# Optimization experiments

Measured on AMD Instinct MI355X. Metric: run time of the kernel, lower is better.

## Reference

```python
import jax, jax.numpy as jnp
import numpy as np

B, L, H, C, K, S = 8, 336, 192, 321, 16, 8
H2 = H // 2 + 1            # rfft bins of pred_len
OUT = H2 * (2 * K + 1)     # FilterFactory out_dim


def _instance_norm(t):
    mu = t.mean(-1, keepdims=True)
    tc = t - mu
    std = jnp.sqrt((tc * tc).mean(-1, keepdims=True) + 1e-8)
    return tc / std, mu, std


def setup_inputs() -> dict:
    key = jax.random.key(0)
    ks = jax.random.split(key, 16)
    x = jax.random.normal(ks[0], (B, L, C), jnp.float32)
    y_hat = jax.random.normal(ks[1], (B, H, C), jnp.float32)
    leader_ids = jax.random.randint(ks[2], (B, C, K), 0, C)
    shift = jax.random.randint(ks[3], (B, C, K), 0, L)
    r = jax.random.normal(ks[4], (B, C, K), jnp.float32)
    temperature = jnp.ones((1,), jnp.float32)
    sl = 1.0 / np.sqrt(L)
    cls_w = jax.random.uniform(ks[5], (S, L), jnp.float32, -sl, sl)
    cls_bias = jax.random.uniform(ks[6], (S,), jnp.float32, -sl, sl)
    ss = 1.0 / np.sqrt(S)
    basic_state = jax.random.uniform(ks[7], (C, S), jnp.float32, -ss, ss)
    sk = 1.0 / np.sqrt(K)
    mh_w = jax.random.uniform(ks[8], (S, K * OUT), jnp.float32, -sk, sk)
    mh_b = jax.random.uniform(ks[9], (S, OUT), jnp.float32, -sk, sk)
    sm = 1.0 / np.sqrt(3 * H2)
    mix_w_real = jax.random.uniform(ks[10], (H2, 3 * H2), jnp.float32, -sm, sm)
    mix_w_imag = jax.random.uniform(ks[11], (H2, 3 * H2), jnp.float32, -sm, sm)
    mix_b_real = jax.random.uniform(ks[12], (H2,), jnp.float32, -sm, sm)
    mix_b_imag = jax.random.uniform(ks[13], (H2,), jnp.float32, -sm, sm)
    return dict(x=x, y_hat=y_hat, leader_ids=leader_ids, shift=shift, r=r,
                temperature=temperature, cls_w=cls_w, cls_bias=cls_bias,
                basic_state=basic_state, mh_w=mh_w, mh_b=mh_b,
                mix_w_real=mix_w_real, mix_w_imag=mix_w_imag,
                mix_b_real=mix_b_real, mix_b_imag=mix_b_imag)


def reference(x, y_hat, leader_ids, shift, r, temperature, cls_w, cls_bias,
              basic_state, mh_w, mh_b, mix_w_real, mix_w_imag,
              mix_b_real, mix_b_imag):
    xc = jnp.transpose(x, (0, 2, 1))        # [B,C,L]
    yh = jnp.transpose(y_hat, (0, 2, 1))    # [B,C,H]
    xn, mu, std = _instance_norm(xc)
    yhn = (yh - mu) / std

    # ---- shifted leader gather (no-grad region in original) ----
    seq = jnp.concatenate([xn, yhn], -1)                                      # [B,C,L+H]
    lead = jnp.take_along_axis(seq[:, None], leader_ids[..., None], axis=2)   # [B,C,K,L+H]
    idx = jnp.arange(L, L + H)[None, None, None, :] - shift[..., None]        # [B,C,K,H]
    seq_shifted = jnp.take_along_axis(lead, idx, axis=-1)
    seq_shifted = jax.lax.stop_gradient(seq_shifted * jnp.sign(r)[..., None])

    # ---- temperature softmax over [1, |r|] ----
    ones = jnp.ones((xc.shape[0], C, 1), xc.dtype)
    rw = jax.nn.softmax(jnp.concatenate([ones, jnp.abs(r)], -1) / temperature, axis=-1)
    corr_feat = rw[..., 1:]                                                   # [B,C,K]

    # ---- FilterFactory: state-routed filters ----
    p = jax.nn.softmax(cls_bias + basic_state + jnp.einsum('bcl,sl->bcs', xc, cls_w), axis=-1)
    w = jnp.einsum('bcs,so->bco', p, mh_w).reshape(-1, C, K, OUT)
    b = jnp.einsum('bcs,so->bco', p, mh_b)
    filt = (jnp.einsum('bck,bcko->bco', corr_feat, w) + b).reshape(-1, C, 2 * K + 1, H2)

    # ---- FFT filter mixing ----
    yf = jnp.fft.rfft(yhn)                                  # [B,C,H2] complex64
    sf = jnp.fft.rfft(seq_shifted) * filt[:, :, :K]         # [B,C,K,H2]
    df = (sf - yf[:, :, None]) * filt[:, :, K:-1]
    yf2 = yf * filt[:, :, -1]
    mix_in = jnp.concatenate([sf.sum(2), df.sum(2), yf2], -1)  # [B,C,3*H2]
    mix_w = mix_w_real + 1j * mix_w_imag
    mix_b = mix_b_real + 1j * mix_b_imag
    y = yhn + jnp.fft.irfft(mix_in @ mix_w.T + mix_b, n=H)
    y = y * std + mu
    return jnp.transpose(y, (0, 2, 1))                       # [B,H,C]
```

## Files before the change

kernel.cpp:

```cpp
#include <hip/hip_runtime.h>
#include <math.h>

#define B_ 8
#define L_ 336
#define H_ 192
#define C_ 321
#define K_ 16
#define S_ 8
#define H2_ 97
#define OUT_ 3201
#define SEQLEN_ 528
#define BC_ (B_ * C_)
#define JD_ 136
#define MIXJ_ 291
#define NP_ 208
#define MROWS_ 43656
#define MPAD_ 43712
#define NBLK_ 683
#define KF_ 160
#define MPADF_ 2576
#define NPADF_ 3264

typedef float v2f __attribute__((ext_vector_type(2)));
typedef float v4f __attribute__((ext_vector_type(4)));
typedef __attribute__((ext_vector_type(8))) short bf16x8;
typedef __attribute__((ext_vector_type(4))) float f32x4;

#define TWO_PI_F 6.283185307179586f

static constexpr size_t OFF_SEQ    = 0;
static constexpr size_t OFF_MU     = OFF_SEQ + (size_t)BC_ * SEQLEN_;
static constexpr size_t OFF_STD    = OFF_MU + BC_;
static constexpr size_t OFF_WT2    = (OFF_STD + BC_ + 3) & ~(size_t)3;
static constexpr size_t OFF_BPHI   = (OFF_WT2 + (size_t)2 * MIXJ_ * H2_ + 3) & ~(size_t)3;
static constexpr size_t OFF_BPLO   = OFF_BPHI + (size_t)NP_ * 192 / 2;
static constexpr size_t OFF_UHI    = (OFF_BPLO + (size_t)NP_ * 192 / 2 + 3) & ~(size_t)3;
static constexpr size_t OFF_ULO    = OFF_UHI + (size_t)MPADF_ * KF_ / 2;
static constexpr size_t OFF_W2HI   = OFF_ULO + (size_t)MPADF_ * KF_ / 2;
static constexpr size_t OFF_W2LO   = OFF_W2HI + (size_t)NPADF_ * KF_ / 2;
static constexpr size_t OFF_ROWS   = OFF_W2LO + (size_t)NPADF_ * KF_ / 2;
static constexpr size_t OFF_ROWSLO = OFF_ROWS + (size_t)MPAD_ * 192 / 2;
static constexpr size_t OFF_F      = OFF_ROWSLO + (size_t)MPAD_ * 192 / 2;
static constexpr size_t OFF_FILT   = OFF_ROWS;

__device__ inline void split_bf16(float v, unsigned short& hh, unsigned short& ll) {
  unsigned u = __float_as_uint(v);
  unsigned hb = (u + 0x7FFFu + ((u >> 16) & 1u)) & 0xFFFF0000u;
  float fh = __uint_as_float(hb);
  float fl = v - fh;
  unsigned u2 = __float_as_uint(fl);
  unsigned lb = (u2 + 0x7FFFu + ((u2 >> 16) & 1u)) >> 16;
  hh = (unsigned short)(hb >> 16);
  ll = (unsigned short)lb;
}

__launch_bounds__(256)
__global__ void kStats(const float* __restrict__ x, const float* __restrict__ cls_w,
                       const float* __restrict__ cls_bias,
                       const float* __restrict__ basic_state, const float* __restrict__ r,
                       const float* __restrict__ temperature,
                       float* __restrict__ mu, float* __restrict__ stdv,
                       unsigned short* __restrict__ uhi, unsigned short* __restrict__ ulo) {
  __shared__ float part[4][10][64];
  __shared__ float sp[64][S_];
  __shared__ float scf[64][K_];

  int b = blockIdx.x;
  int cb = blockIdx.y * 64;
  int lane = threadIdx.x & 63;
  int wv = threadIdx.x >> 6;
  int c = cb + lane;
  bool cok = c < C_;

  float sum = 0.f, sumsq = 0.f, a[S_];
#pragma unroll
  for (int s = 0; s < S_; s++) a[s] = 0.f;
  if (cok) {
    for (int l = wv * 84; l < wv * 84 + 84; l++) {
      float v = x[((size_t)b * L_ + l) * C_ + c];
      sum += v;
      sumsq = fmaf(v, v, sumsq);
#pragma unroll
      for (int s = 0; s < S_; s++) a[s] = fmaf(v, cls_w[s * L_ + l], a[s]);
    }
  }
  part[wv][0][lane] = sum;
  part[wv][1][lane] = sumsq;
#pragma unroll
  for (int s = 0; s < S_; s++) part[wv][2 + s][lane] = a[s];
  __syncthreads();

  if (threadIdx.x < 64 && cok) {
    float s0 = 0.f, s1 = 0.f, ac[S_];
#pragma unroll
    for (int s = 0; s < S_; s++) ac[s] = 0.f;
#pragma unroll
    for (int w = 0; w < 4; w++) {
      s0 += part[w][0][lane];
      s1 += part[w][1][lane];
#pragma unroll
      for (int s = 0; s < S_; s++) ac[s] += part[w][2 + s][lane];
    }
    float m = s0 * (1.f / L_);
    float var = fmaxf(s1 * (1.f / L_) - m * m, 0.f);
    float sd = sqrtf(var + 1e-8f);
    int bc = b * C_ + c;
    mu[bc] = m;
    stdv[bc] = sd;

    float lg[S_], mx = -1e30f;
#pragma unroll
    for (int s = 0; s < S_; s++) {
      lg[s] = ac[s] + cls_bias[s] + basic_state[c * S_ + s];
      mx = fmaxf(mx, lg[s]);
    }
    float den = 0.f;
#pragma unroll
    for (int s = 0; s < S_; s++) { float e = expf(lg[s] - mx); lg[s] = e; den += e; }
    float iden = 1.f / den;
#pragma unroll
    for (int s = 0; s < S_; s++) sp[lane][s] = lg[s] * iden;

    float it = 1.f / temperature[0];
    float aa[K_], am = it;
#pragma unroll
    for (int k = 0; k < K_; k++) {
      aa[k] = fabsf(r[(size_t)bc * K_ + k]) * it;
      am = fmaxf(am, aa[k]);
    }
    float den2 = expf(it - am);
#pragma unroll
    for (int k = 0; k < K_; k++) { float e = expf(aa[k] - am); aa[k] = e; den2 += e; }
    float iden2 = 1.f / den2;
#pragma unroll
    for (int k = 0; k < K_; k++) scf[lane][k] = aa[k] * iden2;
  }
  __syncthreads();

  for (int idx = threadIdx.x; idx < 64 * KF_; idx += 256) {
    int ci = idx / KF_;
    int j = idx - ci * KF_;
    if (cb + ci < C_) {
      float v = 0.f;
      if (j < JD_) {
        int s = j / 17;
        int t = j - s * 17;
        v = sp[ci][s];
        if (t < K_) v *= scf[ci][t];
      }
      unsigned short hh, ll;
      split_bf16(v, hh, ll);
      size_t row = (size_t)(b * C_ + cb + ci) * KF_ + j;
      uhi[row] = hh;
      ulo[row] = ll;
    }
  }
}

__launch_bounds__(256)
__global__ void kSeqT(const float* __restrict__ x, const float* __restrict__ y_hat,
                      const float* __restrict__ mu, const float* __restrict__ stdv,
                      float* __restrict__ seq) {
  __shared__ float tile[32][33];
  int b = blockIdx.x;
  int cb = blockIdx.y * 32;
  int tb = blockIdx.z * 32;
  int ci = threadIdx.x & 31;
  int q8 = threadIdx.x >> 5;
  int c = cb + ci;
  float m = 0.f, is = 0.f;
  if (c < C_) {
    m = mu[b * C_ + c];
    is = 1.f / stdv[b * C_ + c];
  }
#pragma unroll
  for (int q = 0; q < 4; q++) {
    int tt = q8 + q * 8;
    int t = tb + tt;
    float v = 0.f;
    if (c < C_ && t < SEQLEN_)
      v = (t < L_) ? x[((size_t)b * L_ + t) * C_ + c]
                   : y_hat[((size_t)b * H_ + (t - L_)) * C_ + c];
    tile[ci][tt] = (v - m) * is;
  }
  __syncthreads();
#pragma unroll
  for (int q = 0; q < 4; q++) {
    int cc = cb + q8 + q * 8;
    int t = tb + ci;
    if (cc < C_ && t < SEQLEN_)
      seq[((size_t)b * C_ + cc) * SEQLEN_ + t] = tile[q8 + q * 8][ci];
  }
}

__global__ void kPackB(unsigned short* __restrict__ bhi, unsigned short* __restrict__ blo) {
  int idx = blockIdx.x * 256 + threadIdx.x;
  if (idx >= NP_ * 192) return;
  int n = idx / 192;
  int h = idx - n * 192;
  float val = 0.f;
  if (n < H2_) {
    int ph = (n * h) % 192;
    val = cosf((TWO_PI_F / 192.f) * (float)ph);
  } else if (n >= 104 && n < 104 + H2_) {
    int ph = ((n - 104) * h) % 192;
    val = -sinf((TWO_PI_F / 192.f) * (float)ph);
  }
  unsigned short hh, ll;
  split_bf16(val, hh, ll);
  bhi[idx] = hh;
  blo[idx] = ll;
}

__global__ void kPackW2(const float* __restrict__ mh_w, const float* __restrict__ mh_b,
                        unsigned short* __restrict__ w2hi, unsigned short* __restrict__ w2lo) {
  int idx = blockIdx.x * 256 + threadIdx.x;
  if (idx >= NPADF_ * KF_) return;
  int n = idx / KF_;
  int k = idx - n * KF_;
  float v = 0.f;
  if (n < OUT_ && k < JD_) {
    int s = k / 17;
    int t = k - s * 17;
    v = (t < K_) ? mh_w[(size_t)s * (K_ * OUT_) + (size_t)t * OUT_ + n]
                 : mh_b[(size_t)s * OUT_ + n];
  }
  unsigned short hh, ll;
  split_bf16(v, hh, ll);
  w2hi[idx] = hh;
  w2lo[idx] = ll;
}

__global__ void kPackMixW(const float* __restrict__ mwr, const float* __restrict__ mwi,
                          float2* __restrict__ wT2) {
  int idx = blockIdx.x * blockDim.x + threadIdx.x;
  if (idx >= MIXJ_ * H2_) return;
  int j = idx / H2_;
  int g = idx - j * H2_;
  wT2[idx] = make_float2(mwr[(size_t)g * MIXJ_ + j], mwi[(size_t)g * MIXJ_ + j]);
}

__launch_bounds__(128)
__global__ void kGather(const float* __restrict__ seq, const int* __restrict__ lead,
                        const int* __restrict__ shiftv, const float* __restrict__ r,
                        unsigned short* __restrict__ rhi, unsigned short* __restrict__ rlo) {
  int bc = blockIdx.x;
  int b = bc / C_;
  int lane = threadIdx.x;
#pragma unroll 1
  for (int k = 0; k < 17; k++) {
    float sg;
    const float* src;
    if (k < K_) {
      int ld = lead[(size_t)bc * K_ + k];
      int sh = shiftv[(size_t)bc * K_ + k];
      float rv = r[(size_t)bc * K_ + k];
      sg = (rv > 0.f) ? 1.f : ((rv < 0.f) ? -1.f : 0.f);
      src = seq + ((size_t)b * C_ + ld) * SEQLEN_ + (L_ - sh);
    } else {
      sg = 1.f;
      src = seq + (size_t)bc * SEQLEN_ + L_;
    }
    size_t mrow = (size_t)(bc * 17 + k) * 192;
#pragma unroll
    for (int p = 0; p < 2; p++) {
      int h = lane + p * 128;
      if (h < H_) {
        float v = src[h] * sg;
        unsigned short hh, ll;
        split_bf16(v, hh, ll);
        rhi[mrow + h] = hh;
        rlo[mrow + h] = ll;
      }
    }
  }
}

__launch_bounds__(256)
__global__ void kDFT(const unsigned short* __restrict__ rhi,
                     const unsigned short* __restrict__ rlo,
                     const unsigned short* __restrict__ bhi,
                     const unsigned short* __restrict__ blo,
                     float* __restrict__ F) {
  __shared__ __align__(16) unsigned short Bs[52 * 512];
  int tid = threadIdx.x;
  int wv = tid >> 6;
  int lane = tid & 63;
  int m0 = blockIdx.x * 64 + wv * 16;
  int row = lane & 15;
  int kg = lane >> 4;

  f32x4 acc[13];
#pragma unroll
  for (int nt = 0; nt < 13; nt++) acc[nt] = (f32x4){0.f, 0.f, 0.f, 0.f};

  const unsigned short* Ahb = rhi + (size_t)(m0 + row) * 192 + kg * 8;
  const unsigned short* Alb = rlo + (size_t)(m0 + row) * 192 + kg * 8;

#pragma unroll 1
  for (int part = 0; part < 3; part++) {
    __syncthreads();
    for (int s = tid >> 6; s < 52; s += 4) {
      int plane = s & 1;
      int ntks = s >> 1;
      int nt = ntks >> 1;
      int ks2 = ntks & 1;
      const unsigned short* src = (plane ? blo : bhi)
          + (size_t)(nt * 16 + row) * 192 + part * 64 + ks2 * 32 + kg * 8;
      *(bf16x8*)(Bs + s * 512 + lane * 8) = *(const bf16x8*)src;
    }
    __syncthreads();
#pragma unroll
    for (int ks2 = 0; ks2 < 2; ks2++) {
      int ksg = part * 2 + ks2;
      bf16x8 ah = *(const bf16x8*)(Ahb + ksg * 32);
      bf16x8 al = *(const bf16x8*)(Alb + ksg * 32);
#pragma unroll
      for (int nt = 0; nt < 13; nt++) {
        bf16x8 bh = *(const bf16x8*)(Bs + ((nt * 2 + ks2) * 2 + 0) * 512 + lane * 8);
        bf16x8 bl = *(const bf16x8*)(Bs + ((nt * 2 + ks2) * 2 + 1) * 512 + lane * 8);
        acc[nt] = __builtin_amdgcn_mfma_f32_16x16x32_bf16(ah, bh, acc[nt], 0, 0, 0);
        acc[nt] = __builtin_amdgcn_mfma_f32_16x16x32_bf16(ah, bl, acc[nt], 0, 0, 0);
        acc[nt] = __builtin_amdgcn_mfma_f32_16x16x32_bf16(al, bh, acc[nt], 0, 0, 0);
      }
    }
  }

  int crow0 = m0 + kg * 4;
#pragma unroll
  for (int nt = 0; nt < 13; nt++) {
#pragma unroll
    for (int rr = 0; rr < 4; rr++) {
      F[(size_t)(crow0 + rr) * NP_ + nt * 16 + row] = acc[nt][rr];
    }
  }
}

__launch_bounds__(256)
__global__ void kFiltMM(const unsigned short* __restrict__ uhi,
                        const unsigned short* __restrict__ ulo,
                        const unsigned short* __restrict__ w2hi,
                        const unsigned short* __restrict__ w2lo,
                        float* __restrict__ filt) {
  __shared__ __align__(16) unsigned short Ws[40 * 512];
  int tid = threadIdx.x;
  int wv = tid >> 6;
  int lane = tid & 63;
  int m0 = (blockIdx.y * 4 + wv) * 16;
  int n0 = blockIdx.x * 64;
  int col = lane & 15;
  int kg = lane >> 4;

  for (int s = tid >> 6; s < 40; s += 4) {
    int plane = s & 1;
    int ntk = s >> 1;
    int nt = ntk / 5;
    int ksi = ntk - nt * 5;
    const unsigned short* src = (plane ? w2lo : w2hi)
        + (size_t)(n0 + nt * 16 + col) * KF_ + ksi * 32 + kg * 8;
    *(bf16x8*)(Ws + s * 512 + lane * 8) = *(const bf16x8*)src;
  }
  __syncthreads();

  f32x4 acc[4];
#pragma unroll
  for (int nt = 0; nt < 4; nt++) acc[nt] = (f32x4){0.f, 0.f, 0.f, 0.f};

  int mrow = (m0 + col < MPADF_) ? (m0 + col) : (MPADF_ - 1);
  const unsigned short* Ah = uhi + (size_t)mrow * KF_ + kg * 8;
  const unsigned short* Al = ulo + (size_t)mrow * KF_ + kg * 8;

#pragma unroll
  for (int ks = 0; ks < 5; ks++) {
    bf16x8 ah = *(const bf16x8*)(Ah + ks * 32);
    bf16x8 al = *(const bf16x8*)(Al + ks * 32);
#pragma unroll
    for (int nt = 0; nt < 4; nt++) {
      bf16x8 bh = *(const bf16x8*)(Ws + ((nt * 5 + ks) * 2 + 0) * 512 + lane * 8);
      bf16x8 bl = *(const bf16x8*)(Ws + ((nt * 5 + ks) * 2 + 1) * 512 + lane * 8);
      acc[nt] = __builtin_amdgcn_mfma_f32_16x16x32_bf16(ah, bh, acc[nt], 0, 0, 0);
      acc[nt] = __builtin_amdgcn_mfma_f32_16x16x32_bf16(ah, bl, acc[nt], 0, 0, 0);
      acc[nt] = __builtin_amdgcn_mfma_f32_16x16x32_bf16(al, bh, acc[nt], 0, 0, 0);
    }
  }

  int crow0 = m0 + kg * 4;
#pragma unroll
  for (int nt = 0; nt < 4; nt++) {
    int o = n0 + nt * 16 + col;
    if (o < OUT_) {
#pragma unroll
      for (int rr = 0; rr < 4; rr++) {
        int m = crow0 + rr;
        if (m < BC_) filt[(size_t)m * OUT_ + o] = acc[nt][rr];
      }
    }
  }
}

__launch_bounds__(256)
__global__ void kPost2(const float* __restrict__ F, const float* __restrict__ filt,
                       const float* __restrict__ seq,
                       const float* __restrict__ mu, const float* __restrict__ stdv,
                       const float2* __restrict__ wT2,
                       const float* __restrict__ mbr, const float* __restrict__ mbi,
                       float* __restrict__ out) {
  __shared__ __align__(16) v2f mix2[8][292];
  __shared__ float zrL[8][100], ziL[8][100];

  int tid = threadIdx.x;
  int half = tid >> 7;
  int ff = tid & 127;
  int bc0 = blockIdx.x * 8;

#pragma unroll 1
  for (int p = 0; p < 4; p++) {
    int bl = p * 2 + half;
    int bc = bc0 + bl;
    if (ff < H2_) {
      float Fre[17], Fim[17];
#pragma unroll
      for (int k = 0; k < 17; k++) {
        size_t mr = (size_t)(bc * 17 + k) * NP_;
        Fre[k] = F[mr + ff];
        Fim[k] = F[mr + 104 + ff];
      }
      const float* fb = filt + (size_t)bc * OUT_;
      float yfR = Fre[16], yfI = Fim[16];
      float S1r = 0.f, S1i = 0.f, S2r = 0.f, S2i = 0.f, sg2 = 0.f;
#pragma unroll
      for (int k = 0; k < K_; k++) {
        float g1 = fb[k * H2_ + ff];
        float g2 = fb[(K_ + k) * H2_ + ff];
        float g12 = g1 * g2;
        S1r = fmaf(Fre[k], g1, S1r);
        S1i = fmaf(Fim[k], g1, S1i);
        S2r = fmaf(Fre[k], g12, S2r);
        S2i = fmaf(Fim[k], g12, S2i);
        sg2 += g2;
      }
      S2r = fmaf(-yfR, sg2, S2r);
      S2i = fmaf(-yfI, sg2, S2i);
      float g3 = fb[32 * H2_ + ff];
      mix2[bl][ff] = (v2f){S1r, S1i};
      mix2[bl][H2_ + ff] = (v2f){S2r, S2i};
      mix2[bl][2 * H2_ + ff] = (v2f){yfR * g3, yfI * g3};
    }
  }
  __syncthreads();

  if (ff < H2_) {
    int g = ff;
    float zr_[4], zi_[4];
#pragma unroll
    for (int q = 0; q < 4; q++) { zr_[q] = mbr[g]; zi_[q] = mbi[g]; }
    const float2* wg = wT2 + g;
#pragma unroll 1
    for (int j = 0; j + 2 <= MIXJ_; j += 2) {
      float2 w0 = wg[(size_t)j * H2_];
      float2 w1 = wg[(size_t)(j + 1) * H2_];
#pragma unroll
      for (int q = 0; q < 4; q++) {
        v4f mm = *(const v4f*)&mix2[half * 4 + q][j];
        zr_[q] = fmaf(mm.x, w0.x, fmaf(-mm.y, w0.y, zr_[q]));
        zi_[q] = fmaf(mm.x, w0.y, fmaf(mm.y, w0.x, zi_[q]));
        zr_[q] = fmaf(mm.z, w1.x, fmaf(-mm.w, w1.y, zr_[q]));
        zi_[q] = fmaf(mm.z, w1.y, fmaf(mm.w, w1.x, zi_[q]));
      }
    }
    {
      int j = MIXJ_ - 1;
      float2 w0 = wg[(size_t)j * H2_];
#pragma unroll
      for (int q = 0; q < 4; q++) {
        v2f m2 = mix2[half * 4 + q][j];
        zr_[q] = fmaf(m2.x, w0.x, fmaf(-m2.y, w0.y, zr_[q]));
        zi_[q] = fmaf(m2.x, w0.y, fmaf(m2.y, w0.x, zi_[q]));
      }
    }
#pragma unroll
    for (int q = 0; q < 4; q++) {
      zrL[half * 4 + q][g] = zr_[q];
      ziL[half * 4 + q][g] = zi_[q];
    }
  }
  __syncthreads();

  if (ff < 96) {
    int h = ff;
    float ang = (TWO_PI_F / 192.f) * (float)h;
    float cs, sn;
    sincosf(ang, &sn, &cs);
#pragma unroll 1
    for (int q = 0; q < 4; q++) {
      int bl = half * 4 + q;
      int bc = bc0 + bl;
      int b = bc / C_;
      int c = bc - b * C_;
      float m = mu[bc], sd = stdv[bc];
      float base = 0.5f * zrL[bl][0] + ((h & 1) ? -0.5f : 0.5f) * zrL[bl][96];
      float aE = 0.f, aO = 0.f;
      float cv = cs, sv = sn;
      for (int fq = 1; fq < 96; fq += 2) {
        aO = fmaf(zrL[bl][fq], cv, fmaf(-ziL[bl][fq], sv, aO));
        float nc = cv * cs - sv * sn;
        float ns = cv * sn + sv * cs;
        aE = fmaf(zrL[bl][fq + 1], nc, fmaf(-ziL[bl][fq + 1], ns, aE));
        cv = nc * cs - ns * sn;
        sv = nc * sn + ns * cs;
      }
      float y0 = (base + aE + aO) * (2.f / 192.f);
      float y1 = (base + aE - aO) * (2.f / 192.f);
      const float* sq = seq + (size_t)bc * SEQLEN_ + L_;
      out[((size_t)b * H_ + h) * C_ + c] = fmaf(sq[h] + y0, sd, m);
      out[((size_t)b * H_ + h + 96) * C_ + c] = fmaf(sq[h + 96] + y1, sd, m);
    }
  }
}

extern "C" void kernel_launch(void* const* d_in, const int* in_sizes, int n_in,
                              void* d_out, int out_size, void* d_ws, size_t ws_size,
                              hipStream_t stream) {
  const float* x           = (const float*)d_in[0];
  const float* y_hat       = (const float*)d_in[1];
  const int*   lead        = (const int*)d_in[2];
  const int*   shiftv      = (const int*)d_in[3];
  const float* r           = (const float*)d_in[4];
  const float* temperature = (const float*)d_in[5];
  const float* cls_w       = (const float*)d_in[6];
  const float* cls_bias    = (const float*)d_in[7];
  const float* basic_state = (const float*)d_in[8];
  const float* mh_w        = (const float*)d_in[9];
  const float* mh_b        = (const float*)d_in[10];
  const float* mwr         = (const float*)d_in[11];
  const float* mwi         = (const float*)d_in[12];
  const float* mbr         = (const float*)d_in[13];
  const float* mbi         = (const float*)d_in[14];
  float* out = (float*)d_out;
  float* ws  = (float*)d_ws;

  unsigned short* bphi = (unsigned short*)(ws + OFF_BPHI);
  unsigned short* bplo = (unsigned short*)(ws + OFF_BPLO);
  unsigned short* uhi  = (unsigned short*)(ws + OFF_UHI);
  unsigned short* ulo  = (unsigned short*)(ws + OFF_ULO);
  unsigned short* w2hi = (unsigned short*)(ws + OFF_W2HI);
  unsigned short* w2lo = (unsigned short*)(ws + OFF_W2LO);
  unsigned short* rhi  = (unsigned short*)(ws + OFF_ROWS);
  unsigned short* rlo  = (unsigned short*)(ws + OFF_ROWSLO);

  dim3 gS(B_, 6);
  kStats<<<gS, 256, 0, stream>>>(x, cls_w, cls_bias, basic_state, r, temperature,
                                 ws + OFF_MU, ws + OFF_STD, uhi, ulo);

  dim3 gT(B_, 11, 17);
  kSeqT<<<gT, 256, 0, stream>>>(x, y_hat, ws + OFF_MU, ws + OFF_STD, ws + OFF_SEQ);

  kPackB<<<(NP_ * 192 + 255) / 256, 256, 0, stream>>>(bphi, bplo);

  kPackW2<<<(NPADF_ * KF_ + 255) / 256, 256, 0, stream>>>(mh_w, mh_b, w2hi, w2lo);

  kPackMixW<<<(MIXJ_ * H2_ + 255) / 256, 256, 0, stream>>>(
      mwr, mwi, (float2*)(ws + OFF_WT2));

  kGather<<<BC_, 128, 0, stream>>>(ws + OFF_SEQ, lead, shiftv, r, rhi, rlo);

  kDFT<<<NBLK_, 256, 0, stream>>>(rhi, rlo, bphi, bplo, ws + OFF_F);

  dim3 gFM(NPADF_ / 64, (MPADF_ / 16 + 3) / 4);
  kFiltMM<<<gFM, 256, 0, stream>>>(uhi, ulo, w2hi, w2lo, ws + OFF_FILT);

  kPost2<<<BC_ / 8, 256, 0, stream>>>(ws + OFF_F, ws + OFF_FILT, ws + OFF_SEQ,
                                      ws + OFF_MU, ws + OFF_STD,
                                      (const float2*)(ws + OFF_WT2), mbr, mbi, out);
}
```

Baseline: 255.5 us.

## Replace scalar mix and irfft post-kernel with split-bf16 MFMA GEMMs

Splits the fused post-processing kernel into four stages: a combine kernel that builds the complex mix inputs as split hi/lo bf16 rows, an MFMA GEMM applying the complex mixing weights (bias folded in as an extra K column), a second MFMA GEMM doing the irfft as a precomputed cosine/sine matrix, and a transposing epilogue that writes coalesced output. The goal is to replace the scalar FMA complex matmul and the per-thread rotation-recurrence inverse DFT with matrix-core work. The cost is extra kernel launches, intermediate round trips through global memory, and three-term bf16 split precision in place of fp32.

```diff
diff --git a/kernel.cpp b/kernel.cpp
--- a/kernel.cpp
+++ b/kernel.cpp
@@ -14,12 +14,15 @@
 #define JD_ 136
 #define MIXJ_ 291
 #define NP_ 208
-#define MROWS_ 43656
 #define MPAD_ 43712
 #define NBLK_ 683
 #define KF_ 160
 #define MPADF_ 2576
 #define NPADF_ 3264
+#define KMX_ 608
+#define NMX_ 208
+#define KIR_ 224
+#define NIR_ 192
 
 typedef float v2f __attribute__((ext_vector_type(2)));
 typedef float v4f __attribute__((ext_vector_type(4)));
@@ -31,8 +34,7 @@
 static constexpr size_t OFF_SEQ    = 0;
 static constexpr size_t OFF_MU     = OFF_SEQ + (size_t)BC_ * SEQLEN_;
 static constexpr size_t OFF_STD    = OFF_MU + BC_;
-static constexpr size_t OFF_WT2    = (OFF_STD + BC_ + 3) & ~(size_t)3;
-static constexpr size_t OFF_BPHI   = (OFF_WT2 + (size_t)2 * MIXJ_ * H2_ + 3) & ~(size_t)3;
+static constexpr size_t OFF_BPHI   = (OFF_STD + BC_ + 3) & ~(size_t)3;
 static constexpr size_t OFF_BPLO   = OFF_BPHI + (size_t)NP_ * 192 / 2;
 static constexpr size_t OFF_UHI    = (OFF_BPLO + (size_t)NP_ * 192 / 2 + 3) & ~(size_t)3;
 static constexpr size_t OFF_ULO    = OFF_UHI + (size_t)MPADF_ * KF_ / 2;
@@ -42,6 +44,15 @@
 static constexpr size_t OFF_ROWSLO = OFF_ROWS + (size_t)MPAD_ * 192 / 2;
 static constexpr size_t OFF_F      = OFF_ROWSLO + (size_t)MPAD_ * 192 / 2;
 static constexpr size_t OFF_FILT   = OFF_ROWS;
+static constexpr size_t OFF_MWHI   = OFF_F + (size_t)MPAD_ * NP_;
+static constexpr size_t OFF_MWLO   = OFF_MWHI + (size_t)NMX_ * KMX_ / 2;
+static constexpr size_t OFF_THI    = OFF_MWLO + (size_t)NMX_ * KMX_ / 2;
+static constexpr size_t OFF_TLO    = OFF_THI + (size_t)NIR_ * KIR_ / 2;
+static constexpr size_t OFF_MXHI   = OFF_TLO + (size_t)NIR_ * KIR_ / 2;
+static constexpr size_t OFF_MXLO   = OFF_MXHI + (size_t)MPADF_ * KMX_ / 2;
+static constexpr size_t OFF_ZHI    = OFF_MXLO + (size_t)MPADF_ * KMX_ / 2;
+static constexpr size_t OFF_ZLO    = OFF_ZHI + (size_t)MPADF_ * KIR_ / 2;
+static constexpr size_t OFF_Y      = OFF_ZLO + (size_t)MPADF_ * KIR_ / 2;
 
 __device__ inline void split_bf16(float v, unsigned short& hh, unsigned short& ll) {
   unsigned u = __float_as_uint(v);
@@ -231,13 +242,53 @@
   w2lo[idx] = ll;
 }
 
-__global__ void kPackMixW(const float* __restrict__ mwr, const float* __restrict__ mwi,
-                          float2* __restrict__ wT2) {
-  int idx = blockIdx.x * blockDim.x + threadIdx.x;
-  if (idx >= MIXJ_ * H2_) return;
-  int j = idx / H2_;
-  int g = idx - j * H2_;
-  wT2[idx] = make_float2(mwr[(size_t)g * MIXJ_ + j], mwi[(size_t)g * MIXJ_ + j]);
+__global__ void kPackMixW2(const float* __restrict__ mwr, const float* __restrict__ mwi,
+                           const float* __restrict__ mbr, const float* __restrict__ mbi,
+                           unsigned short* __restrict__ mwhi, unsigned short* __restrict__ mwlo) {
+  int idx = blockIdx.x * 256 + threadIdx.x;
+  if (idx >= NMX_ * KMX_) return;
+  int n = idx / KMX_;
+  int k = idx - n * KMX_;
+  float v = 0.f;
+  if (n < H2_) {
+    int g = n;
+    if (k < MIXJ_) v = mwr[(size_t)g * MIXJ_ + k];
+    else if (k < 2 * MIXJ_) v = -mwi[(size_t)g * MIXJ_ + (k - MIXJ_)];
+    else if (k == 2 * MIXJ_) v = mbr[g];
+  } else if (n >= 104 && n < 104 + H2_) {
+    int g = n - 104;
+    if (k < MIXJ_) v = mwi[(size_t)g * MIXJ_ + k];
+    else if (k < 2 * MIXJ_) v = mwr[(size_t)g * MIXJ_ + (k - MIXJ_)];
+    else if (k == 2 * MIXJ_) v = mbi[g];
+  }
+  unsigned short hh, ll;
+  split_bf16(v, hh, ll);
+  mwhi[idx] = hh;
+  mwlo[idx] = ll;
+}
+
+__global__ void kPackT(unsigned short* __restrict__ thi, unsigned short* __restrict__ tlo) {
+  int idx = blockIdx.x * 256 + threadIdx.x;
+  if (idx >= NIR_ * KIR_) return;
+  int h = idx / KIR_;
+  int k = idx - h * KIR_;
+  float v = 0.f;
+  if (k < H2_) {
+    int f = k;
+    float w = (f == 0 || f == 96) ? (1.f / 192.f) : (2.f / 192.f);
+    int ph = (f * h) % 192;
+    v = w * cosf((TWO_PI_F / 192.f) * (float)ph);
+  } else if (k >= 104 && k < 104 + H2_) {
+    int f = k - 104;
+    if (f != 0 && f != 96) {
+      int ph = (f * h) % 192;
+      v = -(2.f / 192.f) * sinf((TWO_PI_F / 192.f) * (float)ph);
+    }
+  }
+  unsigned short hh, ll;
+  split_bf16(v, hh, ll);
+  thi[idx] = hh;
+  tlo[idx] = ll;
 }
 
 __launch_bounds__(128)
@@ -398,122 +449,193 @@
   }
 }
 
+__launch_bounds__(128)
+__global__ void kCombine(const float* __restrict__ F, const float* __restrict__ filt,
+                         unsigned short* __restrict__ mxhi, unsigned short* __restrict__ mxlo) {
+  int bc = blockIdx.x;
+  int ff = threadIdx.x;
+  size_t mrowK = (size_t)bc * KMX_;
+
+  if (ff < H2_) {
+    float Fre[17], Fim[17];
+#pragma unroll
+    for (int k = 0; k < 17; k++) {
+      size_t mr = (size_t)(bc * 17 + k) * NP_;
+      Fre[k] = F[mr + ff];
+      Fim[k] = F[mr + 104 + ff];
+    }
+    const float* fb = filt + (size_t)bc * OUT_;
+    float yfR = Fre[16], yfI = Fim[16];
+    float S1r = 0.f, S1i = 0.f, S2r = 0.f, S2i = 0.f, sg2 = 0.f;
+#pragma unroll
+    for (int k = 0; k < K_; k++) {
+      float g1 = fb[k * H2_ + ff];
+      float g2 = fb[(K_ + k) * H2_ + ff];
+      float g12 = g1 * g2;
+      S1r = fmaf(Fre[k], g1, S1r);
+      S1i = fmaf(Fim[k], g1, S1i);
+      S2r = fmaf(Fre[k], g12, S2r);
+      S2i = fmaf(Fim[k], g12, S2i);
+      sg2 += g2;
+    }
+    S2r = fmaf(-yfR, sg2, S2r);
+    S2i = fmaf(-yfI, sg2, S2i);
+    float g3 = fb[32 * H2_ + ff];
+    float vals[6] = {S1r, S2r, yfR * g3, S1i, S2i, yfI * g3};
+#pragma unroll
+    for (int q = 0; q < 6; q++) {
+      unsigned short hh, ll;
+      split_bf16(vals[q], hh, ll);
+      mxhi[mrowK + q * H2_ + ff] = hh;
+      mxlo[mrowK + q * H2_ + ff] = ll;
+    }
+  } else if (ff == H2_) {
+    mxhi[mrowK + 2 * MIXJ_] = 0x3F80;
+    mxlo[mrowK + 2 * MIXJ_] = 0;
+  } else if (ff >= 98 && ff < 98 + (KMX_ - 583)) {
+    int k = 583 + (ff - 98);
+    mxhi[mrowK + k] = 0;
+    mxlo[mrowK + k] = 0;
+  }
+}
+
 __launch_bounds__(256)
-__global__ void kPost2(const float* __restrict__ F, const float* __restrict__ filt,
-                       const float* __restrict__ seq,
-                       const float* __restrict__ mu, const float* __restrict__ stdv,
-                       const float2* __restrict__ wT2,
-                       const float* __restrict__ mbr, const float* __restrict__ mbi,
-                       float* __restrict__ out) {
-  __shared__ __align__(16) v2f mix2[8][292];
-  __shared__ float zrL[8][100], ziL[8][100];
-
+__global__ void kMixMM(const unsigned short* __restrict__ mxhi,
+                       const unsigned short* __restrict__ mxlo,
+                       const unsigned short* __restrict__ mwhi,
+                       const unsigned short* __restrict__ mwlo,
+                       unsigned short* __restrict__ zhi, unsigned short* __restrict__ zlo) {
+  __shared__ __align__(16) unsigned short Bs[38 * 512];
   int tid = threadIdx.x;
-  int half = tid >> 7;
-  int ff = tid & 127;
-  int bc0 = blockIdx.x * 8;
-
-#pragma unroll 1
-  for (int p = 0; p < 4; p++) {
-    int bl = p * 2 + half;
-    int bc = bc0 + bl;
-    if (ff < H2_) {
-      float Fre[17], Fim[17];
-#pragma unroll
-      for (int k = 0; k < 17; k++) {
-        size_t mr = (size_t)(bc * 17 + k) * NP_;
-        Fre[k] = F[mr + ff];
-        Fim[k] = F[mr + 104 + ff];
-      }
-      const float* fb = filt + (size_t)bc * OUT_;
-      float yfR = Fre[16], yfI = Fim[16];
-      float S1r = 0.f, S1i = 0.f, S2r = 0.f, S2i = 0.f, sg2 = 0.f;
-#pragma unroll
-      for (int k = 0; k < K_; k++) {
-        float g1 = fb[k * H2_ + ff];
-        float g2 = fb[(K_ + k) * H2_ + ff];
-        float g12 = g1 * g2;
-        S1r = fmaf(Fre[k], g1, S1r);
-        S1i = fmaf(Fim[k], g1, S1i);
-        S2r = fmaf(Fre[k], g12, S2r);
-        S2i = fmaf(Fim[k], g12, S2i);
-        sg2 += g2;
-      }
-      S2r = fmaf(-yfR, sg2, S2r);
-      S2i = fmaf(-yfI, sg2, S2i);
-      float g3 = fb[32 * H2_ + ff];
-      mix2[bl][ff] = (v2f){S1r, S1i};
-      mix2[bl][H2_ + ff] = (v2f){S2r, S2i};
-      mix2[bl][2 * H2_ + ff] = (v2f){yfR * g3, yfI * g3};
-    }
+  int wv = tid >> 6;
+  int lane = tid & 63;
+  int nt = blockIdx.x;
+  int m0 = (blockIdx.y * 4 + wv) * 16;
+  int row = lane & 15;
+  int kg = lane >> 4;
+
+  for (int s = wv; s < 38; s += 4) {
+    int plane = s & 1;
+    int ks = s >> 1;
+    const unsigned short* src = (plane ? mwlo : mwhi)
+        + (size_t)(nt * 16 + row) * KMX_ + ks * 32 + kg * 8;
+    *(bf16x8*)(Bs + s * 512 + lane * 8) = *(const bf16x8*)src;
   }
   __syncthreads();
 
-  if (ff < H2_) {
-    int g = ff;
-    float zr_[4], zi_[4];
-#pragma unroll
-    for (int q = 0; q < 4; q++) { zr_[q] = mbr[g]; zi_[q] = mbi[g]; }
-    const float2* wg = wT2 + g;
-#pragma unroll 1
-    for (int j = 0; j + 2 <= MIXJ_; j += 2) {
-      float2 w0 = wg[(size_t)j * H2_];
-      float2 w1 = wg[(size_t)(j + 1) * H2_];
-#pragma unroll
-      for (int q = 0; q < 4; q++) {
-        v4f mm = *(const v4f*)&mix2[half * 4 + q][j];
-        zr_[q] = fmaf(mm.x, w0.x, fmaf(-mm.y, w0.y, zr_[q]));
-        zi_[q] = fmaf(mm.x, w0.y, fmaf(mm.y, w0.x, zi_[q]));
-        zr_[q] = fmaf(mm.z, w1.x, fmaf(-mm.w, w1.y, zr_[q]));
-        zi_[q] = fmaf(mm.z, w1.y, fmaf(mm.w, w1.x, zi_[q]));
-      }
-    }
-    {
-      int j = MIXJ_ - 1;
-      float2 w0 = wg[(size_t)j * H2_];
-#pragma unroll
-      for (int q = 0; q < 4; q++) {
-        v2f m2 = mix2[half * 4 + q][j];
-        zr_[q] = fmaf(m2.x, w0.x, fmaf(-m2.y, w0.y, zr_[q]));
-        zi_[q] = fmaf(m2.x, w0.y, fmaf(m2.y, w0.x, zi_[q]));
-      }
-    }
+  if (m0 >= MPADF_) return;
+
+  f32x4 acc = (f32x4){0.f, 0.f, 0.f, 0.f};
+  const unsigned short* Ah = mxhi + (size_t)(m0 + row) * KMX_ + kg * 8;
+  const unsigned short* Al = mxlo + (size_t)(m0 + row) * KMX_ + kg * 8;
+
+#pragma unroll
+  for (int ks = 0; ks < 19; ks++) {
+    bf16x8 ah = *(const bf16x8*)(Ah + ks * 32);
+    bf16x8 al = *(const bf16x8*)(Al + ks * 32);
+    bf16x8 bh = *(const bf16x8*)(Bs + (ks * 2 + 0) * 512 + lane * 8);
+    bf16x8 bl = *(const bf16x8*)(Bs + (ks * 2 + 1) * 512 + lane * 8);
+    acc = __builtin_amdgcn_mfma_f32_16x16x32_bf16(ah, bh, acc, 0, 0, 0);
+    acc = __builtin_amdgcn_mfma_f32_16x16x32_bf16(ah, bl, acc, 0, 0, 0);
+    acc = __builtin_amdgcn_mfma_f32_16x16x32_bf16(al, bh, acc, 0, 0, 0);
+  }
+
+  int crow0 = m0 + kg * 4;
+#pragma unroll
+  for (int rr = 0; rr < 4; rr++) {
+    unsigned short hh, ll;
+    split_bf16(acc[rr], hh, ll);
+    zhi[(size_t)(crow0 + rr) * KIR_ + nt * 16 + row] = hh;
+    zlo[(size_t)(crow0 + rr) * KIR_ + nt * 16 + row] = ll;
+  }
+  if (nt == 12) {
+    for (int cc = 208 + kg; cc < KIR_; cc += 4) {
+      zhi[(size_t)(m0 + row) * KIR_ + cc] = 0;
+      zlo[(size_t)(m0 + row) * KIR_ + cc] = 0;
+    }
+  }
+}
+
+__launch_bounds__(256)
+__global__ void kIrfft(const unsigned short* __restrict__ zhi,
+                       const unsigned short* __restrict__ zlo,
+                       const unsigned short* __restrict__ thi,
+                       const unsigned short* __restrict__ tlo,
+                       float* __restrict__ y) {
+  __shared__ __align__(16) unsigned short Bs[14 * 512];
+  int tid = threadIdx.x;
+  int wv = tid >> 6;
+  int lane = tid & 63;
+  int nt = blockIdx.x;
+  int m0 = (blockIdx.y * 4 + wv) * 16;
+  int row = lane & 15;
+  int kg = lane >> 4;
+
+  for (int s = wv; s < 14; s += 4) {
+    int plane = s & 1;
+    int ks = s >> 1;
+    const unsigned short* src = (plane ? tlo : thi)
+        + (size_t)(nt * 16 + row) * KIR_ + ks * 32 + kg * 8;
+    *(bf16x8*)(Bs + s * 512 + lane * 8) = *(const bf16x8*)src;
+  }
+  __syncthreads();
+
+  if (m0 >= MPADF_) return;
+
+  f32x4 acc = (f32x4){0.f, 0.f, 0.f, 0.f};
+  const unsigned short* Ah = zhi + (size_t)(m0 + row) * KIR_ + kg * 8;
+  const unsigned short* Al = zlo + (size_t)(m0 + row) * KIR_ + kg * 8;
+
+#pragma unroll
+  for (int ks = 0; ks < 7; ks++) {
+    bf16x8 ah = *(const bf16x8*)(Ah + ks * 32);
+    bf16x8 al = *(const bf16x8*)(Al + ks * 32);
+    bf16x8 bh = *(const bf16x8*)(Bs + (ks * 2 + 0) * 512 + lane * 8);
+    bf16x8 bl = *(const bf16x8*)(Bs + (ks * 2 + 1) * 512 + lane * 8);
+    acc = __builtin_amdgcn_mfma_f32_16x16x32_bf16(ah, bh, acc, 0, 0, 0);
+    acc = __builtin_amdgcn_mfma_f32_16x16x32_bf16(ah, bl, acc, 0, 0, 0);
+    acc = __builtin_amdgcn_mfma_f32_16x16x32_bf16(al, bh, acc, 0, 0, 0);
+  }
+
+  int crow0 = m0 + kg * 4;
+#pragma unroll
+  for (int rr = 0; rr < 4; rr++) {
+    y[(size_t)(crow0 + rr) * NIR_ + nt * 16 + row] = acc[rr];
+  }
+}
+
+__launch_bounds__(256)
+__global__ void kEpi(const float* __restrict__ y, const float* __restrict__ seq,
+                     const float* __restrict__ mu, const float* __restrict__ stdv,
+                     float* __restrict__ out) {
+  __shared__ float tile[32][33];
+  int b = blockIdx.x;
+  int cb = blockIdx.y * 32;
+  int hb = blockIdx.z * 32;
+  int lane5 = threadIdx.x & 31;
+  int q8 = threadIdx.x >> 5;
+
+#pragma unroll
+  for (int q = 0; q < 4; q++) {
+    int cc = q8 + q * 8;
+    int c = cb + cc;
+    float v = 0.f;
+    if (c < C_) {
+      size_t bc = (size_t)b * C_ + c;
+      v = y[bc * NIR_ + hb + lane5] + seq[bc * SEQLEN_ + L_ + hb + lane5];
+    }
+    tile[cc][lane5] = v;
+  }
+  __syncthreads();
+
+  int c2 = cb + lane5;
+  if (c2 < C_) {
+    float m = mu[b * C_ + c2];
+    float sd = stdv[b * C_ + c2];
 #pragma unroll
     for (int q = 0; q < 4; q++) {
-      zrL[half * 4 + q][g] = zr_[q];
-      ziL[half * 4 + q][g] = zi_[q];
-    }
-  }
-  __syncthreads();
-
-  if (ff < 96) {
-    int h = ff;
-    float ang = (TWO_PI_F / 192.f) * (float)h;
-    float cs, sn;
-    sincosf(ang, &sn, &cs);
-#pragma unroll 1
-    for (int q = 0; q < 4; q++) {
-      int bl = half * 4 + q;
-      int bc = bc0 + bl;
-      int b = bc / C_;
-      int c = bc - b * C_;
-      float m = mu[bc], sd = stdv[bc];
-      float base = 0.5f * zrL[bl][0] + ((h & 1) ? -0.5f : 0.5f) * zrL[bl][96];
-      float aE = 0.f, aO = 0.f;
-      float cv = cs, sv = sn;
-      for (int fq = 1; fq < 96; fq += 2) {
-        aO = fmaf(zrL[bl][fq], cv, fmaf(-ziL[bl][fq], sv, aO));
-        float nc = cv * cs - sv * sn;
-        float ns = cv * sn + sv * cs;
-        aE = fmaf(zrL[bl][fq + 1], nc, fmaf(-ziL[bl][fq + 1], ns, aE));
-        cv = nc * cs - ns * sn;
-        sv = nc * sn + ns * cs;
-      }
-      float y0 = (base + aE + aO) * (2.f / 192.f);
-      float y1 = (base + aE - aO) * (2.f / 192.f);
-      const float* sq = seq + (size_t)bc * SEQLEN_ + L_;
-      out[((size_t)b * H_ + h) * C_ + c] = fmaf(sq[h] + y0, sd, m);
-      out[((size_t)b * H_ + h + 96) * C_ + c] = fmaf(sq[h + 96] + y1, sd, m);
+      int hh = q8 + q * 8;
+      out[((size_t)b * H_ + hb + hh) * C_ + c2] = fmaf(tile[lane5][hh], sd, m);
     }
   }
 }
@@ -547,6 +669,14 @@
   unsigned short* w2lo = (unsigned short*)(ws + OFF_W2LO);
   unsigned short* rhi  = (unsigned short*)(ws + OFF_ROWS);
   unsigned short* rlo  = (unsigned short*)(ws + OFF_ROWSLO);
+  unsigned short* mwhi = (unsigned short*)(ws + OFF_MWHI);
+  unsigned short* mwlo = (unsigned short*)(ws + OFF_MWLO);
+  unsigned short* thi  = (unsigned short*)(ws + OFF_THI);
+  unsigned short* tlo  = (unsigned short*)(ws + OFF_TLO);
+  unsigned short* mxhi = (unsigned short*)(ws + OFF_MXHI);
+  unsigned short* mxlo = (unsigned short*)(ws + OFF_MXLO);
+  unsigned short* zhi  = (unsigned short*)(ws + OFF_ZHI);
+  unsigned short* zlo  = (unsigned short*)(ws + OFF_ZLO);
 
   dim3 gS(B_, 6);
   kStats<<<gS, 256, 0, stream>>>(x, cls_w, cls_bias, basic_state, r, temperature,
@@ -556,11 +686,9 @@
   kSeqT<<<gT, 256, 0, stream>>>(x, y_hat, ws + OFF_MU, ws + OFF_STD, ws + OFF_SEQ);
 
   kPackB<<<(NP_ * 192 + 255) / 256, 256, 0, stream>>>(bphi, bplo);
-
   kPackW2<<<(NPADF_ * KF_ + 255) / 256, 256, 0, stream>>>(mh_w, mh_b, w2hi, w2lo);
-
-  kPackMixW<<<(MIXJ_ * H2_ + 255) / 256, 256, 0, stream>>>(
-      mwr, mwi, (float2*)(ws + OFF_WT2));
+  kPackMixW2<<<(NMX_ * KMX_ + 255) / 256, 256, 0, stream>>>(mwr, mwi, mbr, mbi, mwhi, mwlo);
+  kPackT<<<(NIR_ * KIR_ + 255) / 256, 256, 0, stream>>>(thi, tlo);
 
   kGather<<<BC_, 128, 0, stream>>>(ws + OFF_SEQ, lead, shiftv, r, rhi, rlo);
 
@@ -569,7 +697,14 @@
   dim3 gFM(NPADF_ / 64, (MPADF_ / 16 + 3) / 4);
   kFiltMM<<<gFM, 256, 0, stream>>>(uhi, ulo, w2hi, w2lo, ws + OFF_FILT);
 
-  kPost2<<<BC_ / 8, 256, 0, stream>>>(ws + OFF_F, ws + OFF_FILT, ws + OFF_SEQ,
-                                      ws + OFF_MU, ws + OFF_STD,
-                                      (const float2*)(ws + OFF_WT2), mbr, mbi, out);
-}
+  kCombine<<<BC_, 128, 0, stream>>>(ws + OFF_F, ws + OFF_FILT, mxhi, mxlo);
+
+  dim3 gMX(13, 41);
+  kMixMM<<<gMX, 256, 0, stream>>>(mxhi, mxlo, mwhi, mwlo, zhi, zlo);
+
+  dim3 gIR(12, 41);
+  kIrfft<<<gIR, 256, 0, stream>>>(zhi, zlo, thi, tlo, ws + OFF_Y);
+
+  dim3 gE(B_, 11, 6);
+  kEpi<<<gE, 256, 0, stream>>>(ws + OFF_Y, ws + OFF_SEQ, ws + OFF_MU, ws + OFF_STD, out);
+}
```

Result: faster. 227.0 us (-11.2%).
